# Kernel optimization log

Hardware: AMD Instinct MI355X
Metric: run time of the kernel (lower is better)

The kernel has to match this reference:

```python
import jax, jax.numpy as jnp
import numpy as np

NUM_HEADS = 16


def setup_inputs() -> dict:
    key = jax.random.key(0)
    k1, k2, k3 = jax.random.split(key, 3)
    T, B, E = 2048, 2, 1024
    g = jax.random.normal(k1, (T, B, E), dtype=jnp.float32)
    # xavier-ish scaled weights
    W_in = jax.random.normal(k2, (3 * E, E), dtype=jnp.float32) * 0.02
    b_in = jnp.zeros((3 * E,), dtype=jnp.float32)
    W_out = jax.random.normal(k3, (E, E), dtype=jnp.float32) * 0.02
    b_out = jnp.zeros((E,), dtype=jnp.float32)
    return {"g": g, "W_in": W_in, "b_in": b_in, "W_out": W_out, "b_out": b_out}


def reference(g, W_in, b_in, W_out, b_out):
    # self_attention=True, mode='control', eval (dropout inactive), no masks
    T, B, E = g.shape
    H = NUM_HEADS
    hd = E // H
    scaling = hd ** (-0.5)

    qkv = g @ W_in.T + b_in            # [T, B, 3E]
    q, k, v = jnp.split(qkv, 3, axis=-1)
    q = q * scaling

    def to_heads(x):
        # [T, B, E] -> [B*H, T, hd]
        return x.reshape(T, B * H, hd).transpose(1, 0, 2)

    q, k, v = to_heads(q), to_heads(k), to_heads(v)

    w = jnp.einsum('btd,bsd->bts', q, k)          # [B*H, T, T]
    p = jax.nn.softmax(w, axis=-1)                # attn probs
    attn = jnp.einsum('bts,bsd->btd', p, v)       # [B*H, T, hd]

    attn = attn.transpose(1, 0, 2).reshape(T, B, E)
    out = attn @ W_out.T + b_out                  # [T, B, E]

    sample = p  # mode='control' -> sample is the softmax attn probs
    return out, sample
```

## Files before the change

### kernel.cpp

```cpp
#include <hip/hip_runtime.h>

typedef __bf16 bf16;
typedef __attribute__((ext_vector_type(8))) __bf16 bf16x8;
typedef __attribute__((ext_vector_type(4))) float f32x4;

#define MFMA(a, b, c) __builtin_amdgcn_mfma_f32_16x16x32_bf16(a, b, c, 0, 0, 0)

constexpr int T_ = 2048, B_ = 2, E_ = 1024, H_ = 16, HD = 64;
constexpr int BH = B_ * H_;
constexpr int M_ = T_ * B_;
constexpr size_t SEC = (size_t)BH * T_ * HD;

__device__ inline bf16x8 cvt8(const float* p) {
    const float4* q = (const float4*)p;
    float4 a = q[0], b = q[1];
    bf16x8 r;
    r[0] = (bf16)a.x; r[1] = (bf16)a.y; r[2] = (bf16)a.z; r[3] = (bf16)a.w;
    r[4] = (bf16)b.x; r[5] = (bf16)b.y; r[6] = (bf16)b.z; r[7] = (bf16)b.w;
    return r;
}

__global__ __launch_bounds__(256) void qkv_gemm(const float* __restrict__ g,
                                                const float* __restrict__ Win,
                                                const float* __restrict__ bin,
                                                bf16* __restrict__ qkv) {
    __shared__ bf16 As[64][40];
    __shared__ bf16 Bs[64][40];
    const int tid = threadIdx.x;
    const int mbase = blockIdx.y * 64;
    const int nbase = blockIdx.x * 64;
    const int wave = tid >> 6, lane = tid & 63;
    const int quad = lane >> 4, l16 = lane & 15;
    const int wm = (wave >> 1) * 32, wn = (wave & 1) * 32;

    f32x4 acc[2][2] = {};
    const int lrow = tid >> 2, lcol = (tid & 3) * 8;
    const float* ga = g + (size_t)(mbase + lrow) * E_ + lcol;
    const float* gb = Win + (size_t)(nbase + lrow) * E_ + lcol;

    for (int kk = 0; kk < E_; kk += 32) {
        *(bf16x8*)&As[lrow][lcol] = cvt8(ga + kk);
        *(bf16x8*)&Bs[lrow][lcol] = cvt8(gb + kk);
        __syncthreads();
        bf16x8 a0 = *(const bf16x8*)&As[wm + l16][quad * 8];
        bf16x8 a1 = *(const bf16x8*)&As[wm + 16 + l16][quad * 8];
        bf16x8 b0 = *(const bf16x8*)&Bs[wn + l16][quad * 8];
        bf16x8 b1 = *(const bf16x8*)&Bs[wn + 16 + l16][quad * 8];
        acc[0][0] = MFMA(a0, b0, acc[0][0]);
        acc[0][1] = MFMA(a0, b1, acc[0][1]);
        acc[1][0] = MFMA(a1, b0, acc[1][0]);
        acc[1][1] = MFMA(a1, b1, acc[1][1]);
        __syncthreads();
    }
    for (int i = 0; i < 2; i++)
        for (int j = 0; j < 2; j++)
            for (int r = 0; r < 4; r++) {
                int grow = mbase + wm + i * 16 + quad * 4 + r;
                int gcol = nbase + wn + j * 16 + l16;
                float v = acc[i][j][r] + bin[gcol];
                if (gcol < E_) v *= 0.125f;
                int which = gcol >> 10, e = gcol & 1023;
                int h = e >> 6, d = e & 63;
                int t = grow >> 1, b = grow & 1;
                qkv[(size_t)which * SEC + (size_t)(b * H_ + h) * T_ * HD +
                    (size_t)t * HD + d] = (bf16)v;
            }
}

__global__ __launch_bounds__(256) void attn_kernel(bf16* __restrict__ qkv,
                                                   float* __restrict__ p_out) {
    __shared__ bf16 Qs[64][72];
    __shared__ bf16 Ks[64][72];
    __shared__ bf16 Vt[64][72];
    __shared__ float Ps[64][68];
    __shared__ float rsum[64];
    __shared__ float rinv[64];

    const int tid = threadIdx.x;
    const int qt = blockIdx.x, bh = blockIdx.y;
    const int wave = tid >> 6, lane = tid & 63;
    const int quad = lane >> 4, l16 = lane & 15;

    bf16* qb = qkv + (size_t)bh * T_ * HD + (size_t)qt * 64 * HD;
    const bf16* kb = qkv + SEC + (size_t)bh * T_ * HD;
    const bf16* vb = qkv + 2 * SEC + (size_t)bh * T_ * HD;

    for (int rep = 0; rep < 2; rep++) {
        int idx = tid + rep * 256;
        int r = idx >> 3, c = (idx & 7) * 8;
        *(uint4*)&Qs[r][c] = *(const uint4*)(qb + r * HD + c);
    }
    __syncthreads();

    bf16x8 aq0 = *(const bf16x8*)&Qs[wave * 16 + l16][quad * 8];
    bf16x8 aq1 = *(const bf16x8*)&Qs[wave * 16 + l16][32 + quad * 8];

    float rs[4] = {0.f, 0.f, 0.f, 0.f};
    for (int kt = 0; kt < 32; kt++) {
        for (int rep = 0; rep < 2; rep++) {
            int idx = tid + rep * 256;
            int r = idx >> 3, c = (idx & 7) * 8;
            *(uint4*)&Ks[r][c] = *(const uint4*)(kb + (size_t)(kt * 64 + r) * HD + c);
        }
        __syncthreads();
        for (int jn = 0; jn < 4; jn++) {
            f32x4 s = {};
            bf16x8 b0 = *(const bf16x8*)&Ks[jn * 16 + l16][quad * 8];
            bf16x8 b1 = *(const bf16x8*)&Ks[jn * 16 + l16][32 + quad * 8];
            s = MFMA(aq0, b0, s);
            s = MFMA(aq1, b1, s);
            for (int r = 0; r < 4; r++) rs[r] += __expf(s[r]);
        }
        __syncthreads();
    }
    for (int off = 8; off; off >>= 1)
        for (int r = 0; r < 4; r++) rs[r] += __shfl_xor(rs[r], off, 16);
    if (l16 == 0)
        for (int r = 0; r < 4; r++) rsum[wave * 16 + quad * 4 + r] = rs[r];
    __syncthreads();
    if (tid < 64) rinv[tid] = 1.0f / rsum[tid];
    __syncthreads();

    float ri[4];
    for (int r = 0; r < 4; r++) ri[r] = rinv[wave * 16 + quad * 4 + r];

    f32x4 oacc[4] = {};
    for (int kt = 0; kt < 32; kt++) {
        for (int rep = 0; rep < 2; rep++) {
            int idx = tid + rep * 256;
            int r = idx >> 3, c = (idx & 7) * 8;
            *(uint4*)&Ks[r][c] = *(const uint4*)(kb + (size_t)(kt * 64 + r) * HD + c);
            bf16x8 v = *(const bf16x8*)(vb + (size_t)(kt * 64 + r) * HD + c);
            for (int j = 0; j < 8; j++) Vt[c + j][r] = v[j];
        }
        __syncthreads();
        for (int jn = 0; jn < 4; jn++) {
            f32x4 s = {};
            bf16x8 b0 = *(const bf16x8*)&Ks[jn * 16 + l16][quad * 8];
            bf16x8 b1 = *(const bf16x8*)&Ks[jn * 16 + l16][32 + quad * 8];
            s = MFMA(aq0, b0, s);
            s = MFMA(aq1, b1, s);
            for (int r = 0; r < 4; r++)
                Ps[quad * 4 + r + wave * 16][jn * 16 + l16] = __expf(s[r]) * ri[r];
        }
        __syncthreads();
        float* pb = p_out + (size_t)bh * T_ * T_ + (size_t)(qt * 64) * T_ + kt * 64;
        for (int rep = 0; rep < 4; rep++) {
            int idx = tid + rep * 256;
            int r = idx >> 4, c = (idx & 15) * 4;
            *(float4*)(pb + (size_t)r * T_ + c) = *(const float4*)&Ps[r][c];
        }
        bf16x8 a0 = cvt8(&Ps[wave * 16 + l16][quad * 8]);
        bf16x8 a1 = cvt8(&Ps[wave * 16 + l16][32 + quad * 8]);
        for (int jb = 0; jb < 4; jb++) {
            bf16x8 b0 = *(const bf16x8*)&Vt[jb * 16 + l16][quad * 8];
            bf16x8 b1 = *(const bf16x8*)&Vt[jb * 16 + l16][32 + quad * 8];
            oacc[jb] = MFMA(a0, b0, oacc[jb]);
            oacc[jb] = MFMA(a1, b1, oacc[jb]);
        }
        __syncthreads();
    }

    for (int jb = 0; jb < 4; jb++)
        for (int r = 0; r < 4; r++)
            qb[(size_t)(wave * 16 + quad * 4 + r) * HD + jb * 16 + l16] =
                (bf16)oacc[jb][r];
}

__global__ __launch_bounds__(256) void out_gemm(const bf16* __restrict__ attn,
                                                const float* __restrict__ Wout,
                                                const float* __restrict__ bout,
                                                float* __restrict__ out) {
    __shared__ bf16 As[64][40];
    __shared__ bf16 Bs[64][40];
    const int tid = threadIdx.x;
    const int mbase = blockIdx.y * 64;
    const int nbase = blockIdx.x * 64;
    const int wave = tid >> 6, lane = tid & 63;
    const int quad = lane >> 4, l16 = lane & 15;
    const int wm = (wave >> 1) * 32, wn = (wave & 1) * 32;

    f32x4 acc[2][2] = {};
    const int lrow = tid >> 2, lcol = (tid & 3) * 8;
    const int arow = mbase + lrow;
    const int tok_t = arow >> 1, tok_b = arow & 1;
    const float* gb = Wout + (size_t)(nbase + lrow) * E_ + lcol;

    for (int kk = 0; kk < E_; kk += 32) {
        int kc = kk + lcol;
        int h = kc >> 6, d = kc & 63;
        *(uint4*)&As[lrow][lcol] = *(const uint4*)(attn +
            (size_t)(tok_b * H_ + h) * T_ * HD + (size_t)tok_t * HD + d);
        *(bf16x8*)&Bs[lrow][lcol] = cvt8(gb + kk);
        __syncthreads();
        bf16x8 a0 = *(const bf16x8*)&As[wm + l16][quad * 8];
        bf16x8 a1 = *(const bf16x8*)&As[wm + 16 + l16][quad * 8];
        bf16x8 b0 = *(const bf16x8*)&Bs[wn + l16][quad * 8];
        bf16x8 b1 = *(const bf16x8*)&Bs[wn + 16 + l16][quad * 8];
        acc[0][0] = MFMA(a0, b0, acc[0][0]);
        acc[0][1] = MFMA(a0, b1, acc[0][1]);
        acc[1][0] = MFMA(a1, b0, acc[1][0]);
        acc[1][1] = MFMA(a1, b1, acc[1][1]);
        __syncthreads();
    }
    for (int i = 0; i < 2; i++)
        for (int j = 0; j < 2; j++)
            for (int r = 0; r < 4; r++) {
                int grow = mbase + wm + i * 16 + quad * 4 + r;
                int gcol = nbase + wn + j * 16 + l16;
                out[(size_t)grow * E_ + gcol] = acc[i][j][r] + bout[gcol];
            }
}

extern "C" void kernel_launch(void* const* d_in, const int* in_sizes, int n_in,
                              void* d_out, int out_size, void* d_ws, size_t ws_size,
                              hipStream_t stream) {
    const float* g = (const float*)d_in[0];
    const float* Win = (const float*)d_in[1];
    const float* bin = (const float*)d_in[2];
    const float* Wout = (const float*)d_in[3];
    const float* bout = (const float*)d_in[4];

    float* out = (float*)d_out;
    float* p = out + (size_t)M_ * E_;
    bf16* qkv_ws = (bf16*)d_ws;

    qkv_gemm<<<dim3(48, 64), 256, 0, stream>>>(g, Win, bin, qkv_ws);
    attn_kernel<<<dim3(32, 32), 256, 0, stream>>>(qkv_ws, p);
    out_gemm<<<dim3(16, 64), 256, 0, stream>>>(qkv_ws, Wout, bout, out);
}
```

Baseline: 824.8 us.

## Single-pass attention with deferred normalization and larger prefetched QKV GEMM tiles

The attention kernel no longer makes a separate pass over K just to get the softmax row sums. It writes unnormalized exp scores to the probability output, accumulates P·V unnormalized, then rescales O by the inverse sum and re-reads and rescales the stored probability matrix in place. K/V tiles are now prefetched into registers one iteration ahead. The QKV GEMM moves to 128x128 tiles with 4x4 MFMA fragments per wave and register prefetch of the next K slice. This trades the recomputed QK^T pass for an extra read-modify-write of the 512MB fp32 probability tensor. It also relies on exp not overflowing, since no max is subtracted.

Result: slower. 1.035 ms (+25.5%).

```diff
diff --git a/kernel.cpp b/kernel.cpp
--- a/kernel.cpp
+++ b/kernel.cpp
@@ -19,52 +19,78 @@
     r[4] = (bf16)b.x; r[5] = (bf16)b.y; r[6] = (bf16)b.z; r[7] = (bf16)b.w;
     return r;
 }
+__device__ inline bf16x8 cvt8v(const float4& a, const float4& b) {
+    bf16x8 r;
+    r[0] = (bf16)a.x; r[1] = (bf16)a.y; r[2] = (bf16)a.z; r[3] = (bf16)a.w;
+    r[4] = (bf16)b.x; r[5] = (bf16)b.y; r[6] = (bf16)b.z; r[7] = (bf16)b.w;
+    return r;
+}
 
 __global__ __launch_bounds__(256) void qkv_gemm(const float* __restrict__ g,
                                                 const float* __restrict__ Win,
                                                 const float* __restrict__ bin,
                                                 bf16* __restrict__ qkv) {
-    __shared__ bf16 As[64][40];
-    __shared__ bf16 Bs[64][40];
+    __shared__ bf16 As[128][40];
+    __shared__ bf16 Bs[128][40];
     const int tid = threadIdx.x;
-    const int mbase = blockIdx.y * 64;
-    const int nbase = blockIdx.x * 64;
+    const int mbase = blockIdx.y * 128;
+    const int nbase = blockIdx.x * 128;
     const int wave = tid >> 6, lane = tid & 63;
     const int quad = lane >> 4, l16 = lane & 15;
-    const int wm = (wave >> 1) * 32, wn = (wave & 1) * 32;
-
-    f32x4 acc[2][2] = {};
-    const int lrow = tid >> 2, lcol = (tid & 3) * 8;
-    const float* ga = g + (size_t)(mbase + lrow) * E_ + lcol;
-    const float* gb = Win + (size_t)(nbase + lrow) * E_ + lcol;
+    const int wm = (wave >> 1) * 64, wn = (wave & 1) * 64;
+
+    const int srow = tid >> 1, scol = (tid & 1) * 16;
+    const float* ga = g + (size_t)(mbase + srow) * E_ + scol;
+    const float* gb = Win + (size_t)(nbase + srow) * E_ + scol;
+
+    f32x4 acc[4][4] = {};
+    float4 pa[4], pb_[4];
+    pa[0] = *(const float4*)(ga + 0);  pa[1] = *(const float4*)(ga + 4);
+    pa[2] = *(const float4*)(ga + 8);  pa[3] = *(const float4*)(ga + 12);
+    pb_[0] = *(const float4*)(gb + 0); pb_[1] = *(const float4*)(gb + 4);
+    pb_[2] = *(const float4*)(gb + 8); pb_[3] = *(const float4*)(gb + 12);
 
     for (int kk = 0; kk < E_; kk += 32) {
-        *(bf16x8*)&As[lrow][lcol] = cvt8(ga + kk);
-        *(bf16x8*)&Bs[lrow][lcol] = cvt8(gb + kk);
-        __syncthreads();
-        bf16x8 a0 = *(const bf16x8*)&As[wm + l16][quad * 8];
-        bf16x8 a1 = *(const bf16x8*)&As[wm + 16 + l16][quad * 8];
-        bf16x8 b0 = *(const bf16x8*)&Bs[wn + l16][quad * 8];
-        bf16x8 b1 = *(const bf16x8*)&Bs[wn + 16 + l16][quad * 8];
-        acc[0][0] = MFMA(a0, b0, acc[0][0]);
-        acc[0][1] = MFMA(a0, b1, acc[0][1]);
-        acc[1][0] = MFMA(a1, b0, acc[1][0]);
-        acc[1][1] = MFMA(a1, b1, acc[1][1]);
-        __syncthreads();
-    }
-    for (int i = 0; i < 2; i++)
-        for (int j = 0; j < 2; j++)
+        __syncthreads();
+        *(bf16x8*)&As[srow][scol]     = cvt8v(pa[0], pa[1]);
+        *(bf16x8*)&As[srow][scol + 8] = cvt8v(pa[2], pa[3]);
+        *(bf16x8*)&Bs[srow][scol]     = cvt8v(pb_[0], pb_[1]);
+        *(bf16x8*)&Bs[srow][scol + 8] = cvt8v(pb_[2], pb_[3]);
+        if (kk + 32 < E_) {
+            const float* a2 = ga + kk + 32;
+            const float* b2 = gb + kk + 32;
+            pa[0] = *(const float4*)(a2 + 0);  pa[1] = *(const float4*)(a2 + 4);
+            pa[2] = *(const float4*)(a2 + 8);  pa[3] = *(const float4*)(a2 + 12);
+            pb_[0] = *(const float4*)(b2 + 0); pb_[1] = *(const float4*)(b2 + 4);
+            pb_[2] = *(const float4*)(b2 + 8); pb_[3] = *(const float4*)(b2 + 12);
+        }
+        __syncthreads();
+        bf16x8 af[4], bfr[4];
+        for (int i = 0; i < 4; i++)
+            af[i] = *(const bf16x8*)&As[wm + i * 16 + l16][quad * 8];
+        for (int j = 0; j < 4; j++)
+            bfr[j] = *(const bf16x8*)&Bs[wn + j * 16 + l16][quad * 8];
+        for (int i = 0; i < 4; i++)
+            for (int j = 0; j < 4; j++)
+                acc[i][j] = MFMA(af[i], bfr[j], acc[i][j]);
+    }
+
+    float bias[4];
+    for (int j = 0; j < 4; j++) bias[j] = bin[nbase + wn + j * 16 + l16];
+    for (int i = 0; i < 4; i++)
+        for (int j = 0; j < 4; j++) {
+            int gcol = nbase + wn + j * 16 + l16;
+            int which = gcol >> 10, e = gcol & 1023;
+            int h = e >> 6, d = e & 63;
+            float sc = (gcol < E_) ? 0.125f : 1.0f;
             for (int r = 0; r < 4; r++) {
                 int grow = mbase + wm + i * 16 + quad * 4 + r;
-                int gcol = nbase + wn + j * 16 + l16;
-                float v = acc[i][j][r] + bin[gcol];
-                if (gcol < E_) v *= 0.125f;
-                int which = gcol >> 10, e = gcol & 1023;
-                int h = e >> 6, d = e & 63;
                 int t = grow >> 1, b = grow & 1;
+                float v = (acc[i][j][r] + bias[j]) * sc;
                 qkv[(size_t)which * SEC + (size_t)(b * H_ + h) * T_ * HD +
                     (size_t)t * HD + d] = (bf16)v;
             }
+        }
 }
 
 __global__ __launch_bounds__(256) void attn_kernel(bf16* __restrict__ qkv,
@@ -73,8 +99,7 @@
     __shared__ bf16 Ks[64][72];
     __shared__ bf16 Vt[64][72];
     __shared__ float Ps[64][68];
-    __shared__ float rsum[64];
-    __shared__ float rinv[64];
+    __shared__ float rinv_s[64];
 
     const int tid = threadIdx.x;
     const int qt = blockIdx.x, bh = blockIdx.y;
@@ -85,10 +110,17 @@
     const bf16* kb = qkv + SEC + (size_t)bh * T_ * HD;
     const bf16* vb = qkv + 2 * SEC + (size_t)bh * T_ * HD;
 
+    const int r0 = tid >> 3, c0 = (tid & 7) * 8;
     for (int rep = 0; rep < 2; rep++) {
-        int idx = tid + rep * 256;
-        int r = idx >> 3, c = (idx & 7) * 8;
-        *(uint4*)&Qs[r][c] = *(const uint4*)(qb + r * HD + c);
+        int r = r0 + rep * 32;
+        *(uint4*)&Qs[r][c0] = *(const uint4*)(qb + (size_t)r * HD + c0);
+    }
+    uint4 kreg[2];
+    bf16x8 vreg[2];
+    for (int rep = 0; rep < 2; rep++) {
+        int r = r0 + rep * 32;
+        kreg[rep] = *(const uint4*)(kb + (size_t)r * HD + c0);
+        vreg[rep] = *(const bf16x8*)(vb + (size_t)r * HD + c0);
     }
     __syncthreads();
 
@@ -96,55 +128,40 @@
     bf16x8 aq1 = *(const bf16x8*)&Qs[wave * 16 + l16][32 + quad * 8];
 
     float rs[4] = {0.f, 0.f, 0.f, 0.f};
+    f32x4 oacc[4] = {};
+    float* pb0 = p_out + (size_t)bh * T_ * T_ + (size_t)(qt * 64) * T_;
+
     for (int kt = 0; kt < 32; kt++) {
+        __syncthreads();
         for (int rep = 0; rep < 2; rep++) {
-            int idx = tid + rep * 256;
-            int r = idx >> 3, c = (idx & 7) * 8;
-            *(uint4*)&Ks[r][c] = *(const uint4*)(kb + (size_t)(kt * 64 + r) * HD + c);
-        }
-        __syncthreads();
+            int r = r0 + rep * 32;
+            *(uint4*)&Ks[r][c0] = kreg[rep];
+            for (int j = 0; j < 8; j++) Vt[c0 + j][r] = vreg[rep][j];
+        }
+        if (kt + 1 < 32) {
+            for (int rep = 0; rep < 2; rep++) {
+                int r = r0 + rep * 32;
+                kreg[rep] = *(const uint4*)(kb + (size_t)((kt + 1) * 64 + r) * HD + c0);
+                vreg[rep] = *(const bf16x8*)(vb + (size_t)((kt + 1) * 64 + r) * HD + c0);
+            }
+        }
+        __syncthreads();
+
         for (int jn = 0; jn < 4; jn++) {
             f32x4 s = {};
             bf16x8 b0 = *(const bf16x8*)&Ks[jn * 16 + l16][quad * 8];
             bf16x8 b1 = *(const bf16x8*)&Ks[jn * 16 + l16][32 + quad * 8];
             s = MFMA(aq0, b0, s);
             s = MFMA(aq1, b1, s);
-            for (int r = 0; r < 4; r++) rs[r] += __expf(s[r]);
-        }
-        __syncthreads();
-    }
-    for (int off = 8; off; off >>= 1)
-        for (int r = 0; r < 4; r++) rs[r] += __shfl_xor(rs[r], off, 16);
-    if (l16 == 0)
-        for (int r = 0; r < 4; r++) rsum[wave * 16 + quad * 4 + r] = rs[r];
-    __syncthreads();
-    if (tid < 64) rinv[tid] = 1.0f / rsum[tid];
-    __syncthreads();
-
-    float ri[4];
-    for (int r = 0; r < 4; r++) ri[r] = rinv[wave * 16 + quad * 4 + r];
-
-    f32x4 oacc[4] = {};
-    for (int kt = 0; kt < 32; kt++) {
-        for (int rep = 0; rep < 2; rep++) {
-            int idx = tid + rep * 256;
-            int r = idx >> 3, c = (idx & 7) * 8;
-            *(uint4*)&Ks[r][c] = *(const uint4*)(kb + (size_t)(kt * 64 + r) * HD + c);
-            bf16x8 v = *(const bf16x8*)(vb + (size_t)(kt * 64 + r) * HD + c);
-            for (int j = 0; j < 8; j++) Vt[c + j][r] = v[j];
-        }
-        __syncthreads();
-        for (int jn = 0; jn < 4; jn++) {
-            f32x4 s = {};
-            bf16x8 b0 = *(const bf16x8*)&Ks[jn * 16 + l16][quad * 8];
-            bf16x8 b1 = *(const bf16x8*)&Ks[jn * 16 + l16][32 + quad * 8];
-            s = MFMA(aq0, b0, s);
-            s = MFMA(aq1, b1, s);
-            for (int r = 0; r < 4; r++)
-                Ps[quad * 4 + r + wave * 16][jn * 16 + l16] = __expf(s[r]) * ri[r];
-        }
-        __syncthreads();
-        float* pb = p_out + (size_t)bh * T_ * T_ + (size_t)(qt * 64) * T_ + kt * 64;
+            for (int r = 0; r < 4; r++) {
+                float e = __expf(s[r]);
+                rs[r] += e;
+                Ps[wave * 16 + quad * 4 + r][jn * 16 + l16] = e;
+            }
+        }
+        __syncthreads();
+
+        float* pb = pb0 + kt * 64;
         for (int rep = 0; rep < 4; rep++) {
             int idx = tid + rep * 256;
             int r = idx >> 4, c = (idx & 15) * 4;
@@ -158,13 +175,36 @@
             oacc[jb] = MFMA(a0, b0, oacc[jb]);
             oacc[jb] = MFMA(a1, b1, oacc[jb]);
         }
-        __syncthreads();
-    }
+    }
+
+    for (int off = 8; off; off >>= 1)
+        for (int r = 0; r < 4; r++) rs[r] += __shfl_xor(rs[r], off, 16);
+    if (l16 == 0)
+        for (int r = 0; r < 4; r++)
+            rinv_s[wave * 16 + quad * 4 + r] = 1.0f / rs[r];
+    __syncthreads();
+
+    float ri[4];
+    for (int r = 0; r < 4; r++) ri[r] = rinv_s[wave * 16 + quad * 4 + r];
 
     for (int jb = 0; jb < 4; jb++)
         for (int r = 0; r < 4; r++)
             qb[(size_t)(wave * 16 + quad * 4 + r) * HD + jb * 16 + l16] =
-                (bf16)oacc[jb][r];
+                (bf16)(oacc[jb][r] * ri[r]);
+
+    float rw[4];
+    for (int rep = 0; rep < 4; rep++) rw[rep] = rinv_s[(tid >> 4) + rep * 16];
+    for (int kt = 0; kt < 32; kt++) {
+        float* pb = pb0 + kt * 64;
+        for (int rep = 0; rep < 4; rep++) {
+            int idx = tid + rep * 256;
+            int r = idx >> 4, c = (idx & 15) * 4;
+            float4* ap = (float4*)(pb + (size_t)r * T_ + c);
+            float4 x = *ap;
+            x.x *= rw[rep]; x.y *= rw[rep]; x.z *= rw[rep]; x.w *= rw[rep];
+            *ap = x;
+        }
+    }
 }
 
 __global__ __launch_bounds__(256) void out_gemm(const bf16* __restrict__ attn,
@@ -225,7 +265,7 @@
     float* p = out + (size_t)M_ * E_;
     bf16* qkv_ws = (bf16*)d_ws;
 
-    qkv_gemm<<<dim3(48, 64), 256, 0, stream>>>(g, Win, bin, qkv_ws);
+    qkv_gemm<<<dim3(24, 32), 256, 0, stream>>>(g, Win, bin, qkv_ws);
     attn_kernel<<<dim3(32, 32), 256, 0, stream>>>(qkv_ws, p);
     out_gemm<<<dim3(16, 64), 256, 0, stream>>>(qkv_ws, Wout, bout, out);
 }
```
